# Optimization experiments

Measured on AMD Instinct MI355X. Metric: run time of the kernel, lower is better.

Reference implementation:

```python
import jax, jax.numpy as jnp
import numpy as np

N, K, E = 262144, 8, 16
DT = 0.02  # config.delta_time


def _mono(x, w1, b1, w2, b2):
    # monotonic_fun with increasing=False: out_linear(exp(-in_linear(x)))
    return jnp.exp(-(x @ w1.T + b1)) @ w2.T + b2


def _isin(a, b):
    # rowwise torch.isin: a [N,P], b [N,Q] -> [N,P] bool
    return (a[:, :, None] == b[:, None, :]).any(-1)


def _angle_clamp(vec, v, ang):
    # torch.cosine_similarity(v, vec, dim=-1).abs() > ang gate (eps=1e-8)
    num = jnp.einsum('nd,nrd->nr', v, vec)
    den = jnp.maximum(jnp.linalg.norm(v, axis=-1)[:, None] * jnp.linalg.norm(vec, axis=-1), 1e-8)
    keep = jnp.abs(num / den) > ang
    return jnp.where(keep[..., None], vec, 0.0)


def _linear_params(key, fan_in, fan_out):
    a = 1.0 / np.sqrt(fan_in)
    k1, k2 = jax.random.split(key)
    # weightConstraint(min_b=0) clamps weights to >= 0 at init
    w = jnp.maximum(jax.random.uniform(k1, (fan_out, fan_in), minval=-a, maxval=a), 0.0)
    b = jax.random.uniform(k2, (fan_out,), minval=-a, maxval=a)
    return w, b


def _mono_params(key):
    k1, k2 = jax.random.split(key)
    w1, b1 = _linear_params(k1, 1, E)
    w2, b2 = _linear_params(k2, E, 1)
    return w1, b1, w2, b2


def setup_inputs() -> dict:
    key = jax.random.key(0)
    ks = jax.random.split(key, 12)
    ego = jax.random.normal(ks[0], (N, 16), dtype=jnp.float32)
    ego = ego.at[:, 0].set(jnp.arange(N, dtype=jnp.float32))
    # surrounding-vehicle id columns 7..14 as small integer ids (floats)
    ego = ego.at[:, 7:15].set(jax.random.randint(ks[1], (N, 8), 0, 21).astype(jnp.float32))
    nei = jax.random.normal(ks[2], (N, K, 16), dtype=jnp.float32)
    nei = nei.at[:, :, 0].set(jax.random.randint(ks[3], (N, K), 1, 21).astype(jnp.float32))
    border = jax.random.uniform(ks[4], (4,), dtype=jnp.float32) * 10.0 + 1.0
    recording_time = jnp.zeros((N, K, 2), dtype=jnp.float32)
    p_dest = jax.random.uniform(ks[5], (2,), dtype=jnp.float32)  # relu(rand(2))
    angle = jax.nn.sigmoid(jax.random.uniform(ks[6], (1,), dtype=jnp.float32))
    d = {'ego': ego, 'nei': nei, 'border': border, 'recording_time': recording_time,
         'p_dest': p_dest, 'angle': angle}
    for name, kk in (('rep', ks[7]), ('att', ks[8]), ('bor', ks[9]), ('del', ks[10])):
        w1, b1, w2, b2 = _mono_params(kk)
        d[name + '_w1'], d[name + '_b1'], d[name + '_w2'], d[name + '_b2'] = w1, b1, w2, b2
    return d


def reference(ego, nei, border, recording_time, p_dest, angle,
              rep_w1, rep_b1, rep_w2, rep_b2,
              att_w1, att_b1, att_w2, att_b2,
              bor_w1, bor_b1, bor_w2, bor_b2,
              del_w1, del_b1, del_w2, del_b2):
    ang = angle[0]
    v = ego[:, 3:5]                                        # ego velocity [N,2]
    speed = jnp.linalg.norm(v, axis=-1)
    desired = jnp.stack([speed, jnp.zeros_like(speed)], axis=1)
    f_dest = ((p_dest[1] * desired - v) / p_dest[0])[:, None, :]   # [N,1,2]

    nei_id = nei[:, :, 0]                                  # [N,K]
    idx = _isin(nei_id, ego[:, 7:15]) & (nei_id != 0)

    # --- recording_time buffer update (vectorized remain/new/pad concat) ---
    buf_id, buf_ct = recording_time[:, :, 0], recording_time[:, :, 1]
    ifin = _isin(buf_id, nei_id)                           # buffer slots still present
    ct2 = buf_ct + ifin.astype(buf_ct.dtype)               # increment their counts
    ifnew = (~_isin(nei_id, buf_id)) & (nei_id != 0)       # brand-new neighbor ids
    cand = jnp.concatenate([jnp.stack([buf_id, ct2], -1),
                            jnp.stack([nei_id, jnp.ones_like(nei_id)], -1)], axis=1)  # [N,2K,2]
    ar = jnp.arange(K)
    BIG = 1 << 20
    keyord = jnp.concatenate([jnp.where(ifin, ar, BIG), jnp.where(ifnew, ar + K, BIG)], axis=1)
    order = jnp.argsort(keyord, axis=1)[:, :K]             # stable: remain order, then new, then pad
    skey = jnp.take_along_axis(keyord, order, axis=1)
    new_buf = jnp.where((skey < BIG)[..., None],
                        jnp.take_along_axis(cand, order[..., None], axis=1), 1.0)  # pad with ones
    count = new_buf[:, :, 1]                               # [N,K]

    # --- neighbor attraction / repulsion ---
    r = jnp.where(idx[..., None], nei[:, :, 1:3] - ego[:, None, 1:3], 0.0)
    rn = jnp.linalg.norm(r, axis=-1)
    rns = jnp.where(idx, rn, 1.0)                          # safe divisor (masked slots zeroed below)
    dirn = r / rns[..., None]
    f_attr = (_mono(count[..., None], del_w1, del_b1, del_w2, del_b2)
              * _mono(rn[..., None], att_w1, att_b1, att_w2, att_b2) * dirn)
    v_nei = nei[:, :, 3:5]
    b = rn + jnp.sum((r + v_nei * DT) ** 2, -1) - jnp.sum((v_nei * DT) ** 2, -1)
    b = jnp.sqrt(jnp.maximum(jnp.where(idx, b, 1.0), 1e-12)) / 2.0
    f_repu = _mono(b[..., None], rep_w1, rep_b1, rep_w2, rep_b2) * dirn
    f_attr = jnp.where(idx[..., None], f_attr, 0.0)
    f_repu = jnp.where(idx[..., None], f_repu, 0.0)

    # --- border repulsion (y-axis only), select_lane = [0, -1] ---
    rb_all = ego[:, 2:3] - border                          # [N,4]
    rb = jnp.stack([rb_all[:, 0], rb_all[:, -1]], axis=1)  # [N,2]
    rbn = jnp.abs(rb)
    f_by = _mono(rbn[..., None], bor_w1, bor_b1, bor_w2, bor_b2) * (rb / rbn)[..., None]
    f_bor = jnp.concatenate([jnp.zeros_like(f_by), f_by], axis=-1)  # [N,2,2]

    f_destination = _angle_clamp(f_dest, v, ang).sum(1)
    f_neighbors = _angle_clamp(f_attr, v, ang).sum(1) + _angle_clamp(f_repu, v, ang).sum(1)
    f_border = _angle_clamp(f_bor, v, ang).sum(1)
    return jnp.stack([f_destination, f_neighbors, f_border], axis=1)  # [N,3,2]
```

## Files before the change

kernel.cpp:

```cpp
#include <hip/hip_runtime.h>
#include <math.h>

#define EN 16

__device__ __forceinline__ float mono_fast(float x,
    const float* __restrict__ w1, const float* __restrict__ b1,
    const float* __restrict__ w2, const float* __restrict__ b2) {
    float acc = 0.0f;
#pragma unroll
    for (int e = 0; e < EN; ++e) {
        float pre = fmaf(x, w1[e], b1[e]);
        acc = fmaf(__expf(-pre), w2[e], acc);
    }
    return acc + b2[0];
}

extern "C" __global__ void sfm_pre(const float* __restrict__ del_w1,
                                   const float* __restrict__ del_b1,
                                   const float* __restrict__ del_w2,
                                   const float* __restrict__ del_b2,
                                   float* __restrict__ ws) {
    if (threadIdx.x == 0 && blockIdx.x == 0)
        ws[0] = mono_fast(1.0f, del_w1, del_b1, del_w2, del_b2);
}

extern "C" __global__ void __launch_bounds__(256)
sfm_kernel(const float* __restrict__ ego, const float* __restrict__ nei,
           const float* __restrict__ border, const float* __restrict__ rec,
           const float* __restrict__ p_dest, const float* __restrict__ angle,
           const float* __restrict__ rep_w1, const float* __restrict__ rep_b1,
           const float* __restrict__ rep_w2, const float* __restrict__ rep_b2,
           const float* __restrict__ att_w1, const float* __restrict__ att_b1,
           const float* __restrict__ att_w2, const float* __restrict__ att_b2,
           const float* __restrict__ bor_w1, const float* __restrict__ bor_b1,
           const float* __restrict__ bor_w2, const float* __restrict__ bor_b2,
           const float* __restrict__ del_w1, const float* __restrict__ del_b1,
           const float* __restrict__ del_w2, const float* __restrict__ del_b2,
           const float* __restrict__ del1p,
           float* __restrict__ out, int N)
{
    const int gid = blockIdx.x * blockDim.x + threadIdx.x;
    const int n = gid >> 3;
    const int k = gid & 7;
    if (n >= N) return;
    const int lane = threadIdx.x & 63;
    const int gbase = lane & ~7;

    const float* nb = nei + (size_t)n * 128 + (size_t)k * 16;
    float4 na = *(const float4*)nb;
    const float nvyv = nb[4];
    const float nid = na.x;

    float2 rc = *(const float2*)(rec + (size_t)n * 16 + (size_t)k * 2);
    const float bid = rc.x, bct = rc.y;

    unsigned long long zb = __ballot(bid != 0.0f);
    unsigned long long zn = __ballot(nid == 0.0f);

    float cntk, delv;
    if (__builtin_expect((zb | zn) == 0ull, 1)) {
        cntk = 1.0f;
        delv = del1p ? del1p[0]
                     : mono_fast(1.0f, del_w1, del_b1, del_w2, del_b2);
    } else {
        bool fin = (bid == nid);
#pragma unroll
        for (int t = 1; t < 8; ++t)
            fin = fin || (bid == __shfl_xor(nid, t));

        unsigned long long bal = __ballot(fin);
        unsigned finM = (unsigned)((bal >> gbase) & 0xFFull);
        int popcFin = __popc(finM);
        int jsel = 0, cbits = 0;
#pragma unroll
        for (int j = 0; j < 8; ++j) {
            int bit = (finM >> j) & 1;
            if (bit && cbits == k) jsel = j;
            cbits += bit;
        }
        float bctj = __shfl(bct, gbase + jsel);
        cntk = (k < popcFin) ? (bctj + 1.0f) : 1.0f;
        delv = mono_fast(cntk, del_w1, del_b1, del_w2, del_b2);
    }

    const float* er = ego + (size_t)n * 16;
    float4 ea = *(const float4*)(er);
    float4 eb = *(const float4*)(er + 4);
    float4 ec = *(const float4*)(er + 8);
    float4 ed = *(const float4*)(er + 12);
    const float px = ea.y, py = ea.z, vx = ea.w, vy = eb.x;
    const float speed = sqrtf(vx * vx + vy * vy);

    bool match = (nid == eb.w) || (nid == ec.x) || (nid == ec.y) || (nid == ec.z)
              || (nid == ec.w) || (nid == ed.x) || (nid == ed.y) || (nid == ed.z);
    const bool idxk = match && (nid != 0.0f);

    const float ang = angle[0];
    const float p0 = p_dest[0], p1 = p_dest[1];

    float rx = idxk ? (na.y - px) : 0.0f;
    float ry = idxk ? (na.z - py) : 0.0f;
    float rn = sqrtf(rx * rx + ry * ry);
    float rns = idxk ? rn : 1.0f;
    float dx = rx / rns, dy = ry / rns;

    float att = mono_fast(rn, att_w1, att_b1, att_w2, att_b2);
    float sa = delv * att;
    float fax = idxk ? sa * dx : 0.0f;
    float fay = idxk ? sa * dy : 0.0f;

    float nbx = 0.0f, nby = 0.0f;
    {
        float num = vx * fax + vy * fay;
        float fn = sqrtf(fax * fax + fay * fay);
        float den = fmaxf(speed * fn, 1e-8f);
        if (fabsf(num / den) > ang) { nbx += fax; nby += fay; }
    }

    float sxv = na.w * 0.02f, syv = nvyv * 0.02f;
    float ox = rx + sxv, oy = ry + syv;
    float bsum = rn + (ox * ox + oy * oy) - (sxv * sxv + syv * syv);
    float bgate = idxk ? bsum : 1.0f;
    float bb = sqrtf(fmaxf(bgate, 1e-12f)) * 0.5f;
    float rep = mono_fast(bb, rep_w1, rep_b1, rep_w2, rep_b2);
    float frx = idxk ? rep * dx : 0.0f;
    float fry = idxk ? rep * dy : 0.0f;
    {
        float num = vx * frx + vy * fry;
        float fn = sqrtf(frx * frx + fry * fry);
        float den = fmaxf(speed * fn, 1e-8f);
        if (fabsf(num / den) > ang) { nbx += frx; nby += fry; }
    }

    float bsel = (k == 0) ? border[0] : border[3];
    float rb = py - bsel;
    float rbn = fabsf(rb);
    float mb = mono_fast(rbn, bor_w1, bor_b1, bor_w2, bor_b2);
    float fby = mb * (rb / rbn);
    float bory = 0.0f;
    {
        float num = vy * fby;
        float den = fmaxf(speed * fabsf(fby), 1e-8f);
        if ((fabsf(num / den) > ang) && (k < 2)) bory = fby;
    }

#pragma unroll
    for (int m = 1; m < 8; m <<= 1) {
        nbx  += __shfl_xor(nbx,  m);
        nby  += __shfl_xor(nby,  m);
        bory += __shfl_xor(bory, m);
    }

    float fdx = (p1 * speed - vx) / p0;
    float fdy = (0.0f - vy) / p0;
    float fdex = 0.0f, fdey = 0.0f;
    {
        float num = vx * fdx + vy * fdy;
        float fn = sqrtf(fdx * fdx + fdy * fdy);
        float den = fmaxf(speed * fn, 1e-8f);
        if (fabsf(num / den) > ang) { fdex = fdx; fdey = fdy; }
    }

    float wv = (k == 0) ? fdex
             : (k == 1) ? fdey
             : (k == 2) ? nbx
             : (k == 3) ? nby
             : (k == 4) ? 0.0f
             : bory;
    if (k < 6) out[(size_t)n * 6 + k] = wv;
}

extern "C" void kernel_launch(void* const* d_in, const int* in_sizes, int n_in,
                              void* d_out, int out_size, void* d_ws, size_t ws_size,
                              hipStream_t stream) {
    const float* ego    = (const float*)d_in[0];
    const float* nei    = (const float*)d_in[1];
    const float* border = (const float*)d_in[2];
    const float* rec    = (const float*)d_in[3];
    const float* p_dest = (const float*)d_in[4];
    const float* angle  = (const float*)d_in[5];
    const float* rep_w1 = (const float*)d_in[6];
    const float* rep_b1 = (const float*)d_in[7];
    const float* rep_w2 = (const float*)d_in[8];
    const float* rep_b2 = (const float*)d_in[9];
    const float* att_w1 = (const float*)d_in[10];
    const float* att_b1 = (const float*)d_in[11];
    const float* att_w2 = (const float*)d_in[12];
    const float* att_b2 = (const float*)d_in[13];
    const float* bor_w1 = (const float*)d_in[14];
    const float* bor_b1 = (const float*)d_in[15];
    const float* bor_w2 = (const float*)d_in[16];
    const float* bor_b2 = (const float*)d_in[17];
    const float* del_w1 = (const float*)d_in[18];
    const float* del_b1 = (const float*)d_in[19];
    const float* del_w2 = (const float*)d_in[20];
    const float* del_b2 = (const float*)d_in[21];
    float* out = (float*)d_out;

    int N = in_sizes[0] / 16;

    float* del1p = nullptr;
    if (ws_size >= sizeof(float)) {
        del1p = (float*)d_ws;
        sfm_pre<<<1, 64, 0, stream>>>(del_w1, del_b1, del_w2, del_b2, del1p);
    }

    long long threads = (long long)N * 8;
    dim3 grid((unsigned)((threads + 255) / 256));
    sfm_kernel<<<grid, 256, 0, stream>>>(
        ego, nei, border, rec, p_dest, angle,
        rep_w1, rep_b1, rep_w2, rep_b2,
        att_w1, att_b1, att_w2, att_b2,
        bor_w1, bor_b1, bor_w2, bor_b2,
        del_w1, del_b1, del_w2, del_b2,
        del1p, out, N);
}
```

Measured before the change: 254.7 us.

## Process four agents per thread group with double-buffered prefetch loads

Each 8-lane group now handles four agents in sequence instead of one. The next agent's inputs are loaded before the current one is computed, in a two-slot software pipeline. Uniform values (angle, p_dest, border, the del constant) are hoisted and loaded once per thread. The grid shrinks by four, so there are fewer waves and less per-thread setup, at the cost of more registers and less thread-level parallelism for hiding memory latency.

```diff
diff --git a/kernel.cpp b/kernel.cpp
--- a/kernel.cpp
+++ b/kernel.cpp
@@ -22,6 +22,150 @@
                                    float* __restrict__ ws) {
     if (threadIdx.x == 0 && blockIdx.x == 0)
         ws[0] = mono_fast(1.0f, del_w1, del_b1, del_w2, del_b2);
+}
+
+struct AgentIn {
+    float4 na;  float nvy;
+    float2 rc;
+    float4 ea, eb, ec, ed;
+};
+
+__device__ __forceinline__ AgentIn load_agent(
+    const float* __restrict__ nei, const float* __restrict__ rec,
+    const float* __restrict__ ego, int n, int k) {
+    AgentIn s;
+    const float* nb = nei + (size_t)n * 128 + (size_t)k * 16;
+    s.na  = *(const float4*)nb;
+    s.nvy = nb[4];
+    s.rc  = *(const float2*)(rec + (size_t)n * 16 + (size_t)k * 2);
+    const float* er = ego + (size_t)n * 16;
+    s.ea = *(const float4*)(er);
+    s.eb = *(const float4*)(er + 4);
+    s.ec = *(const float4*)(er + 8);
+    s.ed = *(const float4*)(er + 12);
+    return s;
+}
+
+__device__ __forceinline__ void compute_agent(
+    const AgentIn& s, int n, int k, int gbase, bool valid,
+    float ang, float p0, float p1, float b0v, float b3v, float del1,
+    const float* __restrict__ rep_w1, const float* __restrict__ rep_b1,
+    const float* __restrict__ rep_w2, const float* __restrict__ rep_b2,
+    const float* __restrict__ att_w1, const float* __restrict__ att_b1,
+    const float* __restrict__ att_w2, const float* __restrict__ att_b2,
+    const float* __restrict__ bor_w1, const float* __restrict__ bor_b1,
+    const float* __restrict__ bor_w2, const float* __restrict__ bor_b2,
+    const float* __restrict__ del_w1, const float* __restrict__ del_b1,
+    const float* __restrict__ del_w2, const float* __restrict__ del_b2,
+    float* __restrict__ out)
+{
+    const float nid = s.na.x;
+    const float bid = s.rc.x, bct = s.rc.y;
+
+    unsigned long long zb = __ballot(bid != 0.0f);
+    unsigned long long zn = __ballot(nid == 0.0f);
+
+    float cntk, delv;
+    if (__builtin_expect((zb | zn) == 0ull, 1)) {
+        cntk = 1.0f;
+        delv = del1;
+    } else {
+        bool fin = (bid == nid);
+#pragma unroll
+        for (int t = 1; t < 8; ++t)
+            fin = fin || (bid == __shfl_xor(nid, t));
+        unsigned long long bal = __ballot(fin);
+        unsigned finM = (unsigned)((bal >> gbase) & 0xFFull);
+        int popcFin = __popc(finM);
+        int jsel = 0, cbits = 0;
+#pragma unroll
+        for (int j = 0; j < 8; ++j) {
+            int bit = (finM >> j) & 1;
+            if (bit && cbits == k) jsel = j;
+            cbits += bit;
+        }
+        float bctj = __shfl(bct, gbase + jsel);
+        cntk = (k < popcFin) ? (bctj + 1.0f) : 1.0f;
+        delv = mono_fast(cntk, del_w1, del_b1, del_w2, del_b2);
+    }
+
+    const float px = s.ea.y, py = s.ea.z, vx = s.ea.w, vy = s.eb.x;
+    const float speed = sqrtf(vx * vx + vy * vy);
+
+    bool match = (nid == s.eb.w) || (nid == s.ec.x) || (nid == s.ec.y) || (nid == s.ec.z)
+              || (nid == s.ec.w) || (nid == s.ed.x) || (nid == s.ed.y) || (nid == s.ed.z);
+    const bool idxk = match && (nid != 0.0f);
+
+    float rx = idxk ? (s.na.y - px) : 0.0f;
+    float ry = idxk ? (s.na.z - py) : 0.0f;
+    float rn = sqrtf(rx * rx + ry * ry);
+    float rns = idxk ? rn : 1.0f;
+    float dx = rx / rns, dy = ry / rns;
+
+    float att = mono_fast(rn, att_w1, att_b1, att_w2, att_b2);
+    float sa = delv * att;
+    float fax = idxk ? sa * dx : 0.0f;
+    float fay = idxk ? sa * dy : 0.0f;
+
+    float nbx = 0.0f, nby = 0.0f;
+    {
+        float num = vx * fax + vy * fay;
+        float fn = sqrtf(fax * fax + fay * fay);
+        float den = fmaxf(speed * fn, 1e-8f);
+        if (fabsf(num / den) > ang) { nbx += fax; nby += fay; }
+    }
+
+    float sxv = s.na.w * 0.02f, syv = s.nvy * 0.02f;
+    float ox = rx + sxv, oy = ry + syv;
+    float bsum = rn + (ox * ox + oy * oy) - (sxv * sxv + syv * syv);
+    float bgate = idxk ? bsum : 1.0f;
+    float bb = sqrtf(fmaxf(bgate, 1e-12f)) * 0.5f;
+    float rep = mono_fast(bb, rep_w1, rep_b1, rep_w2, rep_b2);
+    float frx = idxk ? rep * dx : 0.0f;
+    float fry = idxk ? rep * dy : 0.0f;
+    {
+        float num = vx * frx + vy * fry;
+        float fn = sqrtf(frx * frx + fry * fry);
+        float den = fmaxf(speed * fn, 1e-8f);
+        if (fabsf(num / den) > ang) { nbx += frx; nby += fry; }
+    }
+
+    float bsel = (k == 0) ? b0v : b3v;
+    float rb = py - bsel;
+    float rbn = fabsf(rb);
+    float mb = mono_fast(rbn, bor_w1, bor_b1, bor_w2, bor_b2);
+    float fby = mb * (rb / rbn);
+    float bory = 0.0f;
+    {
+        float num = vy * fby;
+        float den = fmaxf(speed * fabsf(fby), 1e-8f);
+        if ((fabsf(num / den) > ang) && (k < 2)) bory = fby;
+    }
+
+#pragma unroll
+    for (int m = 1; m < 8; m <<= 1) {
+        nbx  += __shfl_xor(nbx,  m);
+        nby  += __shfl_xor(nby,  m);
+        bory += __shfl_xor(bory, m);
+    }
+
+    float fdx = (p1 * speed - vx) / p0;
+    float fdy = (0.0f - vy) / p0;
+    float fdex = 0.0f, fdey = 0.0f;
+    {
+        float num = vx * fdx + vy * fdy;
+        float fn = sqrtf(fdx * fdx + fdy * fdy);
+        float den = fmaxf(speed * fn, 1e-8f);
+        if (fabsf(num / den) > ang) { fdex = fdx; fdey = fdy; }
+    }
+
+    float wv = (k == 0) ? fdex
+             : (k == 1) ? fdey
+             : (k == 2) ? nbx
+             : (k == 3) ? nby
+             : (k == 4) ? 0.0f
+             : bory;
+    if (valid && k < 6) out[(size_t)n * 6 + k] = wv;
 }
 
 extern "C" __global__ void __launch_bounds__(256)
@@ -40,134 +184,40 @@
            float* __restrict__ out, int N)
 {
     const int gid = blockIdx.x * blockDim.x + threadIdx.x;
-    const int n = gid >> 3;
+    const int g = gid >> 3;
     const int k = gid & 7;
-    if (n >= N) return;
+    const int n0 = g * 4;
+    if (n0 >= N) return;
     const int lane = threadIdx.x & 63;
     const int gbase = lane & ~7;
 
-    const float* nb = nei + (size_t)n * 128 + (size_t)k * 16;
-    float4 na = *(const float4*)nb;
-    const float nvyv = nb[4];
-    const float nid = na.x;
-
-    float2 rc = *(const float2*)(rec + (size_t)n * 16 + (size_t)k * 2);
-    const float bid = rc.x, bct = rc.y;
-
-    unsigned long long zb = __ballot(bid != 0.0f);
-    unsigned long long zn = __ballot(nid == 0.0f);
-
-    float cntk, delv;
-    if (__builtin_expect((zb | zn) == 0ull, 1)) {
-        cntk = 1.0f;
-        delv = del1p ? del1p[0]
-                     : mono_fast(1.0f, del_w1, del_b1, del_w2, del_b2);
-    } else {
-        bool fin = (bid == nid);
-#pragma unroll
-        for (int t = 1; t < 8; ++t)
-            fin = fin || (bid == __shfl_xor(nid, t));
-
-        unsigned long long bal = __ballot(fin);
-        unsigned finM = (unsigned)((bal >> gbase) & 0xFFull);
-        int popcFin = __popc(finM);
-        int jsel = 0, cbits = 0;
-#pragma unroll
-        for (int j = 0; j < 8; ++j) {
-            int bit = (finM >> j) & 1;
-            if (bit && cbits == k) jsel = j;
-            cbits += bit;
-        }
-        float bctj = __shfl(bct, gbase + jsel);
-        cntk = (k < popcFin) ? (bctj + 1.0f) : 1.0f;
-        delv = mono_fast(cntk, del_w1, del_b1, del_w2, del_b2);
-    }
-
-    const float* er = ego + (size_t)n * 16;
-    float4 ea = *(const float4*)(er);
-    float4 eb = *(const float4*)(er + 4);
-    float4 ec = *(const float4*)(er + 8);
-    float4 ed = *(const float4*)(er + 12);
-    const float px = ea.y, py = ea.z, vx = ea.w, vy = eb.x;
-    const float speed = sqrtf(vx * vx + vy * vy);
-
-    bool match = (nid == eb.w) || (nid == ec.x) || (nid == ec.y) || (nid == ec.z)
-              || (nid == ec.w) || (nid == ed.x) || (nid == ed.y) || (nid == ed.z);
-    const bool idxk = match && (nid != 0.0f);
-
     const float ang = angle[0];
     const float p0 = p_dest[0], p1 = p_dest[1];
-
-    float rx = idxk ? (na.y - px) : 0.0f;
-    float ry = idxk ? (na.z - py) : 0.0f;
-    float rn = sqrtf(rx * rx + ry * ry);
-    float rns = idxk ? rn : 1.0f;
-    float dx = rx / rns, dy = ry / rns;
-
-    float att = mono_fast(rn, att_w1, att_b1, att_w2, att_b2);
-    float sa = delv * att;
-    float fax = idxk ? sa * dx : 0.0f;
-    float fay = idxk ? sa * dy : 0.0f;
-
-    float nbx = 0.0f, nby = 0.0f;
-    {
-        float num = vx * fax + vy * fay;
-        float fn = sqrtf(fax * fax + fay * fay);
-        float den = fmaxf(speed * fn, 1e-8f);
-        if (fabsf(num / den) > ang) { nbx += fax; nby += fay; }
-    }
-
-    float sxv = na.w * 0.02f, syv = nvyv * 0.02f;
-    float ox = rx + sxv, oy = ry + syv;
-    float bsum = rn + (ox * ox + oy * oy) - (sxv * sxv + syv * syv);
-    float bgate = idxk ? bsum : 1.0f;
-    float bb = sqrtf(fmaxf(bgate, 1e-12f)) * 0.5f;
-    float rep = mono_fast(bb, rep_w1, rep_b1, rep_w2, rep_b2);
-    float frx = idxk ? rep * dx : 0.0f;
-    float fry = idxk ? rep * dy : 0.0f;
-    {
-        float num = vx * frx + vy * fry;
-        float fn = sqrtf(frx * frx + fry * fry);
-        float den = fmaxf(speed * fn, 1e-8f);
-        if (fabsf(num / den) > ang) { nbx += frx; nby += fry; }
-    }
-
-    float bsel = (k == 0) ? border[0] : border[3];
-    float rb = py - bsel;
-    float rbn = fabsf(rb);
-    float mb = mono_fast(rbn, bor_w1, bor_b1, bor_w2, bor_b2);
-    float fby = mb * (rb / rbn);
-    float bory = 0.0f;
-    {
-        float num = vy * fby;
-        float den = fmaxf(speed * fabsf(fby), 1e-8f);
-        if ((fabsf(num / den) > ang) && (k < 2)) bory = fby;
-    }
-
-#pragma unroll
-    for (int m = 1; m < 8; m <<= 1) {
-        nbx  += __shfl_xor(nbx,  m);
-        nby  += __shfl_xor(nby,  m);
-        bory += __shfl_xor(bory, m);
-    }
-
-    float fdx = (p1 * speed - vx) / p0;
-    float fdy = (0.0f - vy) / p0;
-    float fdex = 0.0f, fdey = 0.0f;
-    {
-        float num = vx * fdx + vy * fdy;
-        float fn = sqrtf(fdx * fdx + fdy * fdy);
-        float den = fmaxf(speed * fn, 1e-8f);
-        if (fabsf(num / den) > ang) { fdex = fdx; fdey = fdy; }
-    }
-
-    float wv = (k == 0) ? fdex
-             : (k == 1) ? fdey
-             : (k == 2) ? nbx
-             : (k == 3) ? nby
-             : (k == 4) ? 0.0f
-             : bory;
-    if (k < 6) out[(size_t)n * 6 + k] = wv;
+    const float b0v = border[0], b3v = border[3];
+    const float del1 = del1p ? del1p[0]
+                             : mono_fast(1.0f, del_w1, del_b1, del_w2, del_b2);
+    const int nmax = N - 1;
+
+    AgentIn sA = load_agent(nei, rec, ego, min(n0 + 0, nmax), k);
+    AgentIn sB = load_agent(nei, rec, ego, min(n0 + 1, nmax), k);
+
+    compute_agent(sA, n0 + 0, k, gbase, (n0 + 0) < N, ang, p0, p1, b0v, b3v, del1,
+                  rep_w1, rep_b1, rep_w2, rep_b2, att_w1, att_b1, att_w2, att_b2,
+                  bor_w1, bor_b1, bor_w2, bor_b2, del_w1, del_b1, del_w2, del_b2, out);
+    sA = load_agent(nei, rec, ego, min(n0 + 2, nmax), k);
+
+    compute_agent(sB, n0 + 1, k, gbase, (n0 + 1) < N, ang, p0, p1, b0v, b3v, del1,
+                  rep_w1, rep_b1, rep_w2, rep_b2, att_w1, att_b1, att_w2, att_b2,
+                  bor_w1, bor_b1, bor_w2, bor_b2, del_w1, del_b1, del_w2, del_b2, out);
+    sB = load_agent(nei, rec, ego, min(n0 + 3, nmax), k);
+
+    compute_agent(sA, n0 + 2, k, gbase, (n0 + 2) < N, ang, p0, p1, b0v, b3v, del1,
+                  rep_w1, rep_b1, rep_w2, rep_b2, att_w1, att_b1, att_w2, att_b2,
+                  bor_w1, bor_b1, bor_w2, bor_b2, del_w1, del_b1, del_w2, del_b2, out);
+
+    compute_agent(sB, n0 + 3, k, gbase, (n0 + 3) < N, ang, p0, p1, b0v, b3v, del1,
+                  rep_w1, rep_b1, rep_w2, rep_b2, att_w1, att_b1, att_w2, att_b2,
+                  bor_w1, bor_b1, bor_w2, bor_b2, del_w1, del_b1, del_w2, del_b2, out);
 }
 
 extern "C" void kernel_launch(void* const* d_in, const int* in_sizes, int n_in,
@@ -205,7 +255,8 @@
         sfm_pre<<<1, 64, 0, stream>>>(del_w1, del_b1, del_w2, del_b2, del1p);
     }
 
-    long long threads = (long long)N * 8;
+    long long groups = (N + 3) / 4;
+    long long threads = groups * 8;
     dim3 grid((unsigned)((threads + 255) / 256));
     sfm_kernel<<<grid, 256, 0, stream>>>(
         ego, nei, border, rec, p_dest, angle,
```

Measured after the change: 265.2 us. 4.1% more time.
